# Kernel tuning notes

Hardware: AMD Instinct MI355X
Metric: run time of the kernel (lower is better)

## Reference

```python
import jax, jax.numpy as jnp
import numpy as np

DIM = 768
GP_NUM = 49


def setup_inputs() -> dict:
    key = jax.random.key(0)
    ks = jax.random.split(key, 7)
    b, n, d = 16, 1024, DIM
    s = d ** -0.5
    x = jax.random.normal(ks[0], (b, n, d), dtype=jnp.float32)
    W_qkv = jax.random.normal(ks[1], (d, 3 * d), dtype=jnp.float32) * s
    b_qkv = jnp.zeros((3 * d,), dtype=jnp.float32)
    W_proj = jax.random.normal(ks[2], (d, d), dtype=jnp.float32) * s
    b_proj = jnp.zeros((d,), dtype=jnp.float32)
    W_gp = jax.random.normal(ks[3], (d, GP_NUM), dtype=jnp.float32) * s
    alpha = jnp.zeros((1,), dtype=jnp.float32)
    return {"x": x, "W_qkv": W_qkv, "b_qkv": b_qkv, "W_proj": W_proj,
            "b_proj": b_proj, "W_gp": W_gp, "alpha": alpha}


def reference(x, W_qkv, b_qkv, W_proj, b_proj, W_gp, alpha):
    d = x.shape[-1]
    scale = d ** -0.5
    qkv = x @ W_qkv + b_qkv                      # (b, n, 3d)
    q, k, v = jnp.split(qkv, 3, axis=-1)
    scores = jnp.einsum('bnd,bmd->bnm', q, k) * scale
    attn = jax.nn.softmax(scores, axis=-1)       # (b, n, n)
    gw = jax.nn.softmax(q @ W_gp, axis=-1)       # (b, n, gp_num)
    group = jnp.einsum('bng,bmg->bnm', gw, gw)   # (b, n, n)
    a = jax.nn.sigmoid(alpha)                    # (1,)
    weights = attn * (a + (1.0 - a) * group)
    out = jnp.einsum('bnm,bmd->bnd', weights, v)
    return out @ W_proj + b_proj
```

## Files before the change

### kernel.cpp

```cpp
#include <hip/hip_runtime.h>
#include <stdint.h>

typedef __attribute__((ext_vector_type(8))) short short8;
typedef __attribute__((ext_vector_type(4))) short short4v;
typedef __attribute__((ext_vector_type(4))) float floatx4;
typedef _Float16 half2v __attribute__((ext_vector_type(2)));

__device__ __forceinline__ float b2f(unsigned short u) {
  union { unsigned int i; float f; } v; v.i = ((unsigned int)u) << 16; return v.f;
}
__device__ __forceinline__ unsigned short f2b(float f) {
  union { float f; unsigned int i; } v; v.f = f;
  unsigned int i = v.i;
  return (unsigned short)((i + 0x7FFFu + ((i >> 16) & 1u)) >> 16);
}
__device__ __forceinline__ short4v pack4(float a, float b, float c, float d) {
  short4v r;
  r[0] = (short)f2b(a); r[1] = (short)f2b(b); r[2] = (short)f2b(c); r[3] = (short)f2b(d);
  return r;
}

__device__ __forceinline__ void stage16(const unsigned short* g, unsigned short* lds_base) {
  __builtin_amdgcn_global_load_lds((__attribute__((address_space(1))) const unsigned int*)g,
                                   (__attribute__((address_space(3))) unsigned int*)lds_base,
                                   16, 0, 0);
}

template<int SYT, int SXT>
__global__ __launch_bounds__(256, 4) void gemm_bt(
    const unsigned short* __restrict__ A, const unsigned short* __restrict__ B,
    unsigned short* __restrict__ Cb, float* __restrict__ Cf,
    const float* __restrict__ rowdiv, const float* __restrict__ bias,
    int K, int lda, int ldb, int ldc,
    long long sA, long long sB, long long sC, long long sRD)
{
  const int tid  = threadIdx.x;
  const int lane = tid & 63;
  const int wave = tid >> 6;
  const int wr = wave >> 1, wc = wave & 1;
  int m0, n0;
  if constexpr (SYT > 0) {
    const int lin  = blockIdx.x;
    const int xcd  = lin & 7;
    const int rem  = lin >> 3;
    const int yloc = rem / SXT;
    const int x    = rem - yloc * SXT;
    m0 = (xcd * SYT + yloc) * 128;
    n0 = x * 128;
  } else {
    m0 = blockIdx.y * 128;
    n0 = blockIdx.x * 128;
  }
  const int bz = blockIdx.z;
  A += (long long)bz * sA;
  B += (long long)bz * sB;
  const float* rd = rowdiv ? rowdiv + (long long)bz * sRD : (const float*)0;

  __shared__ unsigned short As[128 * 32];
  __shared__ unsigned short Bs[128 * 32];

  floatx4 acc[4][4];
#pragma unroll
  for (int i = 0; i < 4; ++i)
#pragma unroll
    for (int j = 0; j < 4; ++j) acc[i][j] = floatx4{0.f, 0.f, 0.f, 0.f};

  const int t    = (lane & 7) ^ (lane >> 3);
  const int srow = 2 * (lane >> 3) + (t >> 2);
  const int scol = (t & 3) * 8;
  const unsigned short* ga0 = A + (long long)(m0 + wave * 32 + srow) * lda + scol;
  const unsigned short* ga1 = ga0 + 16LL * lda;
  const unsigned short* gb0 = B + (long long)(n0 + wave * 32 + srow) * ldb + scol;
  const unsigned short* gb1 = gb0 + 16LL * ldb;
  unsigned short* lA0 = As + wave * 1024;
  unsigned short* lA1 = lA0 + 512;
  unsigned short* lB0 = Bs + wave * 1024;
  unsigned short* lB1 = lB0 + 512;

  const int l15  = lane & 15;
  const int q    = lane >> 4;
  const int rofs = (l15 >> 1) * 64 + (((q + 4 * (l15 & 1)) ^ (l15 >> 1)) * 8);

  for (int kt = 0; kt < K; kt += 32) {
    __syncthreads();
    stage16(ga0 + kt, lA0);
    stage16(ga1 + kt, lA1);
    stage16(gb0 + kt, lB0);
    stage16(gb1 + kt, lB1);
    __syncthreads();
    short8 af[4], bfv[4];
#pragma unroll
    for (int i = 0; i < 4; ++i) af[i]  = *(const short8*)&As[(wr * 32 + i * 8) * 64 + rofs];
#pragma unroll
    for (int j = 0; j < 4; ++j) bfv[j] = *(const short8*)&Bs[(wc * 32 + j * 8) * 64 + rofs];
#pragma unroll
    for (int i = 0; i < 4; ++i)
#pragma unroll
      for (int j = 0; j < 4; ++j)
        acc[i][j] = __builtin_amdgcn_mfma_f32_16x16x32_bf16(bfv[j], af[i], acc[i][j], 0, 0, 0);
  }

#pragma unroll
  for (int i = 0; i < 4; ++i) {
    const int row = m0 + wr * 64 + i * 16 + l15;
    const float rcp = rd ? __builtin_amdgcn_rcpf(rd[row]) : 1.0f;
#pragma unroll
    for (int j = 0; j < 4; ++j) {
      const int colb = n0 + wc * 64 + j * 16 + q * 4;
      floatx4 v = acc[i][j];
      if (rd) { v[0] *= rcp; v[1] *= rcp; v[2] *= rcp; v[3] *= rcp; }
      if (bias) {
        const float4 bi = *(const float4*)&bias[colb];
        v[0] += bi.x; v[1] += bi.y; v[2] += bi.z; v[3] += bi.w;
      }
      if (Cb) *(short4v*)&Cb[(long long)bz * sC + (long long)row * ldc + colb] = pack4(v[0], v[1], v[2], v[3]);
      else    *(floatx4*)&Cf[(long long)bz * sC + (long long)row * ldc + colb] = v;
    }
  }
}

__global__ __launch_bounds__(256) void score_weights(
    const unsigned short* __restrict__ qkv, const unsigned short* __restrict__ gw,
    unsigned short* __restrict__ Wout, float* __restrict__ L,
    const float* __restrict__ alpha)
{
  const int tid  = threadIdx.x;
  const int lane = tid & 63;
  const int wave = tid >> 6;
  const int wr = wave >> 1, wc = wave & 1;
  const int n0 = blockIdx.x * 128;
  const int m0 = blockIdx.y * 128;
  const int b  = blockIdx.z;

  const int l15 = lane & 15;
  const int q   = lane >> 4;
  const int q8  = q * 8;

  const unsigned short* gq = gw + ((long long)(b * 1024 + m0 + wr * 64)) * 64;
  const unsigned short* gk = gw + ((long long)(b * 1024 + n0 + wc * 64)) * 64;
  floatx4 gacc[4][4];
#pragma unroll
  for (int i = 0; i < 4; ++i)
#pragma unroll
    for (int j = 0; j < 4; ++j) gacc[i][j] = floatx4{0.f, 0.f, 0.f, 0.f};
#pragma unroll
  for (int ks = 0; ks < 2; ++ks) {
    short8 af[4], bfv[4];
#pragma unroll
    for (int i = 0; i < 4; ++i) af[i]  = *(const short8*)&gq[(long long)(i * 16 + l15) * 64 + ks * 32 + q8];
#pragma unroll
    for (int j = 0; j < 4; ++j) bfv[j] = *(const short8*)&gk[(long long)(j * 16 + l15) * 64 + ks * 32 + q8];
#pragma unroll
    for (int i = 0; i < 4; ++i)
#pragma unroll
      for (int j = 0; j < 4; ++j)
        gacc[i][j] = __builtin_amdgcn_mfma_f32_16x16x32_bf16(bfv[j], af[i], gacc[i][j], 0, 0, 0);
  }
  const float aa    = 1.0f / (1.0f + __expf(-alpha[0]));
  const float onema = 1.0f - aa;
  half2v gfp[4][4][2];
#pragma unroll
  for (int i = 0; i < 4; ++i)
#pragma unroll
    for (int j = 0; j < 4; ++j) {
      gfp[i][j][0] = half2v{(_Float16)(aa + onema * gacc[i][j][0]),
                            (_Float16)(aa + onema * gacc[i][j][1])};
      gfp[i][j][1] = half2v{(_Float16)(aa + onema * gacc[i][j][2]),
                            (_Float16)(aa + onema * gacc[i][j][3])};
    }

  const unsigned short* Aq = qkv + ((long long)(b * 1024 + m0)) * 1536;
  const unsigned short* Bk = qkv + ((long long)(b * 1024 + n0)) * 1536 + 768;

  __shared__ unsigned short As[128 * 32];
  __shared__ unsigned short Bs[128 * 32];

  floatx4 sacc[4][4];
#pragma unroll
  for (int i = 0; i < 4; ++i)
#pragma unroll
    for (int j = 0; j < 4; ++j) sacc[i][j] = floatx4{0.f, 0.f, 0.f, 0.f};

  const int t    = (lane & 7) ^ (lane >> 3);
  const int srow = 2 * (lane >> 3) + (t >> 2);
  const int scol = (t & 3) * 8;
  const unsigned short* ga0 = Aq + (long long)(wave * 32 + srow) * 1536 + scol;
  const unsigned short* ga1 = ga0 + 16LL * 1536;
  const unsigned short* gb0 = Bk + (long long)(wave * 32 + srow) * 1536 + scol;
  const unsigned short* gb1 = gb0 + 16LL * 1536;
  unsigned short* lA0 = As + wave * 1024;
  unsigned short* lA1 = lA0 + 512;
  unsigned short* lB0 = Bs + wave * 1024;
  unsigned short* lB1 = lB0 + 512;

  const int rofs = (l15 >> 1) * 64 + (((q + 4 * (l15 & 1)) ^ (l15 >> 1)) * 8);

  for (int kt = 0; kt < 768; kt += 32) {
    __syncthreads();
    stage16(ga0 + kt, lA0);
    stage16(ga1 + kt, lA1);
    stage16(gb0 + kt, lB0);
    stage16(gb1 + kt, lB1);
    __syncthreads();
    short8 af[4], bfv[4];
#pragma unroll
    for (int i = 0; i < 4; ++i) af[i]  = *(const short8*)&As[(wr * 32 + i * 8) * 64 + rofs];
#pragma unroll
    for (int j = 0; j < 4; ++j) bfv[j] = *(const short8*)&Bs[(wc * 32 + j * 8) * 64 + rofs];
#pragma unroll
    for (int i = 0; i < 4; ++i)
#pragma unroll
      for (int j = 0; j < 4; ++j)
        sacc[i][j] = __builtin_amdgcn_mfma_f32_16x16x32_bf16(bfv[j], af[i], sacc[i][j], 0, 0, 0);
  }

  const float scale = 0.03608439182435161f;
  unsigned short* Wb = Wout + ((long long)b << 20);

#pragma unroll
  for (int i = 0; i < 4; ++i) {
    const int row = m0 + wr * 64 + i * 16 + l15;
    float ls = 0.0f;
#pragma unroll
    for (int j = 0; j < 4; ++j) {
      const int colb = n0 + wc * 64 + j * 16 + q * 4;
      float e0 = __expf(sacc[i][j][0] * scale);
      float e1 = __expf(sacc[i][j][1] * scale);
      float e2 = __expf(sacc[i][j][2] * scale);
      float e3 = __expf(sacc[i][j][3] * scale);
      ls += (e0 + e1) + (e2 + e3);
      *(short4v*)&Wb[(long long)row * 1024 + colb] =
        pack4(e0 * (float)gfp[i][j][0][0], e1 * (float)gfp[i][j][0][1],
              e2 * (float)gfp[i][j][1][0], e3 * (float)gfp[i][j][1][1]);
    }
    ls += __shfl_xor(ls, 16, 64);
    ls += __shfl_xor(ls, 32, 64);
    if (lane < 16) atomicAdd(&L[b * 1024 + row], ls);
  }
}

__global__ __launch_bounds__(256) void gw_mfma(
    const unsigned short* __restrict__ qkv, const unsigned short* __restrict__ Wgp64,
    unsigned short* __restrict__ gw)
{
  const int lane = threadIdx.x & 63;
  const int wave = threadIdx.x >> 6;
  const int l15  = lane & 15;
  const int q    = lane >> 4;
  const int q8   = q * 8;
  const long long row0 = (long long)blockIdx.x * 64 + wave * 16;
  const unsigned short* A = qkv + row0 * 1536;

  floatx4 acc[4];
#pragma unroll
  for (int j = 0; j < 4; ++j) acc[j] = floatx4{0.f, 0.f, 0.f, 0.f};

  for (int kt = 0; kt < 768; kt += 32) {
    short8 af = *(const short8*)&A[(long long)l15 * 1536 + kt + q8];
    short8 bf[4];
#pragma unroll
    for (int j = 0; j < 4; ++j)
      bf[j] = *(const short8*)&Wgp64[(j * 16 + l15) * 768 + kt + q8];
#pragma unroll
    for (int j = 0; j < 4; ++j)
      acc[j] = __builtin_amdgcn_mfma_f32_16x16x32_bf16(bf[j], af, acc[j], 0, 0, 0);
  }

  float mx = -1e30f;
#pragma unroll
  for (int j = 0; j < 4; ++j)
#pragma unroll
    for (int e = 0; e < 4; ++e) {
      const int col = j * 16 + q * 4 + e;
      if (col < 49) mx = fmaxf(mx, acc[j][e]);
    }
  mx = fmaxf(mx, __shfl_xor(mx, 16, 64));
  mx = fmaxf(mx, __shfl_xor(mx, 32, 64));

  float ev[4][4];
  float s = 0.0f;
#pragma unroll
  for (int j = 0; j < 4; ++j)
#pragma unroll
    for (int e = 0; e < 4; ++e) {
      const int col = j * 16 + q * 4 + e;
      const float x = (col < 49) ? __expf(acc[j][e] - mx) : 0.0f;
      ev[j][e] = x;
      s += x;
    }
  s += __shfl_xor(s, 16, 64);
  s += __shfl_xor(s, 32, 64);
  const float inv = 1.0f / s;

  unsigned short* out = gw + (row0 + l15) * 64;
#pragma unroll
  for (int j = 0; j < 4; ++j)
    *(short4v*)&out[j * 16 + q * 4] =
      pack4(ev[j][0] * inv, ev[j][1] * inv, ev[j][2] * inv, ev[j][3] * inv);
}

__global__ __launch_bounds__(256) void small_gemm_nt(
    const unsigned short* __restrict__ A, const unsigned short* __restrict__ B,
    unsigned short* __restrict__ C)
{
  const int lane = threadIdx.x & 63;
  const int wave = threadIdx.x >> 6;
  const int l15  = lane & 15;
  const int q    = lane >> 4;
  const int q8   = q * 8;
  const int rows0 = (blockIdx.y * 4 + wave) * 16;
  const int cols0 = blockIdx.x * 64;

  floatx4 acc[4];
#pragma unroll
  for (int j = 0; j < 4; ++j) acc[j] = floatx4{0.f, 0.f, 0.f, 0.f};

  for (int kt = 0; kt < 768; kt += 32) {
    short8 af = *(const short8*)&A[(rows0 + l15) * 768 + kt + q8];
    short8 bf[4];
#pragma unroll
    for (int j = 0; j < 4; ++j)
      bf[j] = *(const short8*)&B[(cols0 + j * 16 + l15) * 768 + kt + q8];
#pragma unroll
    for (int j = 0; j < 4; ++j)
      acc[j] = __builtin_amdgcn_mfma_f32_16x16x32_bf16(bf[j], af, acc[j], 0, 0, 0);
  }

  unsigned short* out = C + (rows0 + l15) * 768 + cols0;
#pragma unroll
  for (int j = 0; j < 4; ++j)
    *(short4v*)&out[j * 16 + q * 4] = pack4(acc[j][0], acc[j][1], acc[j][2], acc[j][3]);
}

__global__ void convert_f2b(const float* __restrict__ in, unsigned short* __restrict__ out, long long n)
{
  long long i = ((long long)blockIdx.x * 256 + threadIdx.x) * 4;
  if (i + 3 >= n) {
    for (long long k = i; k < n; ++k) out[k] = f2b(in[k]);
    return;
  }
  float4 v = *(const float4*)(in + i);
  out[i + 0] = f2b(v.x);
  out[i + 1] = f2b(v.y);
  out[i + 2] = f2b(v.z);
  out[i + 3] = f2b(v.w);
}

__global__ void transpose_f2b(const float* __restrict__ in, unsigned short* __restrict__ out,
                              int R, int C, int ldin, int ldout)
{
  __shared__ unsigned short t[32][33];
  const int c0 = blockIdx.x * 32, r0 = blockIdx.y * 32;
  for (int i = threadIdx.y; i < 32; i += 8) {
    const int r = r0 + i, c = c0 + threadIdx.x;
    if (r < R && c < C) t[i][threadIdx.x] = f2b(in[(long long)r * ldin + c]);
  }
  __syncthreads();
  for (int i = threadIdx.y; i < 32; i += 8) {
    const int r = c0 + i, c = r0 + threadIdx.x;
    if (r < C && c < R) out[(long long)r * ldout + c] = t[threadIdx.x][i];
  }
}

__global__ void slice_f2b(const float* __restrict__ in, unsigned short* __restrict__ out)
{
  const long long idx = (long long)blockIdx.x * 256 + threadIdx.x;
  const int r = (int)(idx / 768), c = (int)(idx - (long long)r * 768);
  out[idx] = f2b(in[(long long)r * 2304 + 1536 + c]);
}

__global__ __launch_bounds__(256) void bias2_kernel(
    const unsigned short* __restrict__ WprojT, const float* __restrict__ b_qkv,
    const float* __restrict__ b_proj, float* __restrict__ bias2)
{
  const int lane = threadIdx.x & 63;
  const int wave = threadIdx.x >> 6;
  const int j = blockIdx.x * 4 + wave;
  float s = 0.0f;
#pragma unroll
  for (int tt = 0; tt < 12; ++tt) {
    const int d = tt * 64 + lane;
    s += b2f(WprojT[j * 768 + d]) * b_qkv[1536 + d];
  }
#pragma unroll
  for (int m = 1; m < 64; m <<= 1) s += __shfl_xor(s, m, 64);
  if (lane == 0) bias2[j] = b_proj[j] + s;
}

extern "C" void kernel_launch(void* const* d_in, const int* in_sizes, int n_in,
                              void* d_out, int out_size, void* d_ws, size_t ws_size,
                              hipStream_t stream)
{
  const float* x      = (const float*)d_in[0];
  const float* W_qkv  = (const float*)d_in[1];
  const float* b_qkv  = (const float*)d_in[2];
  const float* W_proj = (const float*)d_in[3];
  const float* b_proj = (const float*)d_in[4];
  const float* W_gp   = (const float*)d_in[5];
  const float* alpha  = (const float*)d_in[6];

  char* p = (char*)d_ws;
  auto alloc = [&](size_t bytes) { char* r = p; p += (bytes + 255) & ~255ULL; return r; };
  unsigned short* qk     = (unsigned short*)alloc(16384ULL * 1536 * 2);
  unsigned short* xb     = (unsigned short*)alloc(16384ULL * 768 * 2);
  unsigned short* WqkvT  = (unsigned short*)alloc(1536ULL * 768 * 2);
  unsigned short* WprojT = (unsigned short*)alloc(768ULL * 768 * 2);
  unsigned short* WvB    = (unsigned short*)alloc(768ULL * 768 * 2);
  unsigned short* Wcomb  = (unsigned short*)alloc(768ULL * 768 * 2);
  unsigned short* Wgp64  = (unsigned short*)alloc(64ULL * 768 * 2);
  unsigned short* gwbuf  = (unsigned short*)alloc(16384ULL * 64 * 2);
  float*          Lbuf   = (float*)alloc(16384ULL * 4);
  float*          bias2  = (float*)alloc(768ULL * 4);
  unsigned short* wmat   = (unsigned short*)alloc(16ULL * 1024 * 1024 * 2);
  unsigned short* vpT    = (unsigned short*)alloc(16ULL * 768 * 1024 * 2);

  const dim3 blk256(256);
  const dim3 tb(32, 8);

  convert_f2b<<<dim3(12288), blk256, 0, stream>>>(x, xb, 16384LL * 768);
  transpose_f2b<<<dim3(48, 24), tb, 0, stream>>>(W_qkv, WqkvT, 768, 1536, 2304, 768);
  transpose_f2b<<<dim3(24, 24), tb, 0, stream>>>(W_proj, WprojT, 768, 768, 768, 768);
  hipMemsetAsync(Wgp64, 0, 64ULL * 768 * 2, stream);
  transpose_f2b<<<dim3(2, 24), tb, 0, stream>>>(W_gp, Wgp64, 768, 49, 49, 768);
  slice_f2b<<<dim3(2304), blk256, 0, stream>>>(W_qkv, WvB);

  small_gemm_nt<<<dim3(12, 12), blk256, 0, stream>>>(WprojT, WvB, Wcomb);
  bias2_kernel<<<dim3(192), blk256, 0, stream>>>(WprojT, b_qkv, b_proj, bias2);

  gemm_bt<16, 12><<<dim3(1536, 1, 1), blk256, 0, stream>>>(xb, WqkvT, qk, (float*)0,
                                                           (const float*)0, b_qkv,
                                                           768, 768, 768, 1536, 0, 0, 0, 0);

  gw_mfma<<<dim3(256), blk256, 0, stream>>>(qk, Wgp64, gwbuf);

  hipMemsetAsync(Lbuf, 0, 16384 * 4, stream);

  score_weights<<<dim3(8, 8, 16), blk256, 0, stream>>>(qk, gwbuf, wmat, Lbuf, alpha);

  gemm_bt<0, 0><<<dim3(8, 6, 16), blk256, 0, stream>>>(Wcomb, xb, vpT, (float*)0,
                                                       (const float*)0, (const float*)0,
                                                       768, 768, 768, 1024,
                                                       0, 1024LL * 768, 768LL * 1024, 0);

  gemm_bt<0, 0><<<dim3(6, 8, 16), blk256, 0, stream>>>(wmat, vpT, (unsigned short*)0, (float*)d_out,
                                                       Lbuf, bias2,
                                                       1024, 1024, 1024, 768,
                                                       1024LL * 1024, 768LL * 1024, 1024LL * 768, 1024);
}
```

Measured before the change: 366.8 us.

## Split QKV GEMM between 128-tile kernel and new 256x256-tile 512-thread kernel

Adds a 256x256-tile GEMM kernel with 512 threads, a 4-stage global_load_lds pipeline and XCD-aware block mapping. The QKV projection is split in half: the first 8192 rows still use the existing 128-tile kernel, and the second half uses the new large-tile kernel. Larger tiles raise data reuse per LDS load, but they also mean fewer blocks (192) and higher register and LDS pressure, and the two halves run one after the other on the stream.

```diff
diff --git a/kernel.cpp b/kernel.cpp
--- a/kernel.cpp
+++ b/kernel.cpp
@@ -119,6 +119,125 @@
   }
 }
 
+template<int SYT, int SXT>
+__global__ __launch_bounds__(512, 1) void gemm256d(
+    const unsigned short* __restrict__ A, const unsigned short* __restrict__ B,
+    unsigned short* __restrict__ Cb, float* __restrict__ Cf,
+    const float* __restrict__ rowdiv, const float* __restrict__ bias,
+    int K, int lda, int ldb, int ldc,
+    long long sA, long long sB, long long sC, long long sRD)
+{
+  const int tid  = threadIdx.x;
+  const int lane = tid & 63;
+  const int wave = tid >> 6;
+  const int wr = wave >> 2;
+  const int wc = wave & 3;
+  int m0, n0;
+  if constexpr (SYT > 0) {
+    const int lin  = blockIdx.x;
+    const int xcd  = lin & 7;
+    const int rem  = lin >> 3;
+    const int yloc = rem / SXT;
+    const int x    = rem - yloc * SXT;
+    m0 = (xcd * SYT + yloc) * 256;
+    n0 = x * 256;
+  } else {
+    m0 = blockIdx.y * 256;
+    n0 = blockIdx.x * 256;
+  }
+  const int bz = blockIdx.z;
+  A += (long long)bz * sA;
+  B += (long long)bz * sB;
+  const float* rd = rowdiv ? rowdiv + (long long)bz * sRD : (const float*)0;
+
+  __shared__ __align__(16) unsigned short lds[4 * 16384];
+
+  floatx4 acc[8][4];
+#pragma unroll
+  for (int i = 0; i < 8; ++i)
+#pragma unroll
+    for (int j = 0; j < 4; ++j) acc[i][j] = floatx4{0.f, 0.f, 0.f, 0.f};
+
+  const int t    = (lane & 7) ^ (lane >> 3);
+  const int srow = 2 * (lane >> 3) + (t >> 2);
+  const int scol = (t & 3) * 8;
+  const unsigned short* ga0 = A + (long long)(m0 + wave * 32 + srow) * lda + scol;
+  const unsigned short* ga1 = ga0 + 16LL * lda;
+  const unsigned short* gb0 = B + (long long)(n0 + wave * 32 + srow) * ldb + scol;
+  const unsigned short* gb1 = gb0 + 16LL * ldb;
+
+  const int l15  = lane & 15;
+  const int q    = lane >> 4;
+  const int rofs = (l15 >> 1) * 64 + (((q + 4 * (l15 & 1)) ^ (l15 >> 1)) * 8);
+
+  short8 af8[8], bfv[4];
+
+  auto STAGE = [&](int kt, int buf) {
+    unsigned short* dA = lds + buf * 16384 + wave * 1024;
+    unsigned short* dB = dA + 8192;
+    stage16(ga0 + kt, dA);
+    stage16(ga1 + kt, dA + 512);
+    stage16(gb0 + kt, dB);
+    stage16(gb1 + kt, dB + 512);
+  };
+  auto READ_ALL = [&](int buf) {
+    const unsigned short* Ab = lds + buf * 16384;
+    const unsigned short* Bb = Ab + 8192;
+#pragma unroll
+    for (int j = 0; j < 4; ++j)
+      bfv[j] = *(const short8*)&Bb[(wc * 32 + j * 8) * 64 + rofs];
+#pragma unroll
+    for (int i = 0; i < 8; ++i)
+      af8[i] = *(const short8*)&Ab[(wr * 64 + i * 8) * 64 + rofs];
+  };
+  auto MFMA32 = [&]() {
+#pragma unroll
+    for (int i = 0; i < 8; ++i)
+#pragma unroll
+      for (int j = 0; j < 4; ++j)
+        acc[i][j] = __builtin_amdgcn_mfma_f32_16x16x32_bf16(bfv[j], af8[i], acc[i][j], 0, 0, 0);
+  };
+
+  const int nt = K >> 5;
+
+  STAGE(0, 0);
+  STAGE(32, 1);
+  STAGE(64, 2);
+  asm volatile("s_waitcnt vmcnt(8)" ::: "memory");
+  __builtin_amdgcn_s_barrier();
+
+  for (int tt = 0; tt < nt; ++tt) {
+    const int buf = tt & 3;
+    if (tt + 3 < nt) STAGE((tt + 3) << 5, (tt + 3) & 3);
+    READ_ALL(buf);
+    __builtin_amdgcn_s_setprio(1);
+    MFMA32();
+    __builtin_amdgcn_s_setprio(0);
+    if (tt < nt - 3)       { asm volatile("s_waitcnt vmcnt(8)" ::: "memory"); }
+    else if (tt == nt - 3) { asm volatile("s_waitcnt vmcnt(4)" ::: "memory"); }
+    else if (tt == nt - 2) { asm volatile("s_waitcnt vmcnt(0)" ::: "memory"); }
+    if (tt + 1 < nt) __builtin_amdgcn_s_barrier();
+  }
+
+#pragma unroll
+  for (int i = 0; i < 8; ++i) {
+    const int row = m0 + wr * 128 + i * 16 + l15;
+    const float rcp = rd ? __builtin_amdgcn_rcpf(rd[row]) : 1.0f;
+#pragma unroll
+    for (int j = 0; j < 4; ++j) {
+      const int colb = n0 + wc * 64 + j * 16 + q * 4;
+      floatx4 v = acc[i][j];
+      if (rd) { v[0] *= rcp; v[1] *= rcp; v[2] *= rcp; v[3] *= rcp; }
+      if (bias) {
+        const float4 bi = *(const float4*)&bias[colb];
+        v[0] += bi.x; v[1] += bi.y; v[2] += bi.z; v[3] += bi.w;
+      }
+      if (Cb) *(short4v*)&Cb[(long long)bz * sC + (long long)row * ldc + colb] = pack4(v[0], v[1], v[2], v[3]);
+      else    *(floatx4*)&Cf[(long long)bz * sC + (long long)row * ldc + colb] = v;
+    }
+  }
+}
+
 __global__ __launch_bounds__(256) void score_weights(
     const unsigned short* __restrict__ qkv, const unsigned short* __restrict__ gw,
     unsigned short* __restrict__ Wout, float* __restrict__ L,
@@ -415,6 +534,7 @@
   unsigned short* vpT    = (unsigned short*)alloc(16ULL * 768 * 1024 * 2);
 
   const dim3 blk256(256);
+  const dim3 blk512(512);
   const dim3 tb(32, 8);
 
   convert_f2b<<<dim3(12288), blk256, 0, stream>>>(x, xb, 16384LL * 768);
@@ -427,9 +547,13 @@
   small_gemm_nt<<<dim3(12, 12), blk256, 0, stream>>>(WprojT, WvB, Wcomb);
   bias2_kernel<<<dim3(192), blk256, 0, stream>>>(WprojT, b_qkv, b_proj, bias2);
 
-  gemm_bt<16, 12><<<dim3(1536, 1, 1), blk256, 0, stream>>>(xb, WqkvT, qk, (float*)0,
-                                                           (const float*)0, b_qkv,
-                                                           768, 768, 768, 1536, 0, 0, 0, 0);
+  gemm_bt<8, 12><<<dim3(768, 1, 1), blk256, 0, stream>>>(xb, WqkvT, qk, (float*)0,
+                                                         (const float*)0, b_qkv,
+                                                         768, 768, 768, 1536, 0, 0, 0, 0);
+  gemm256d<4, 6><<<dim3(192, 1, 1), blk512, 0, stream>>>(xb + 8192LL * 768, WqkvT,
+                                                         qk + 8192LL * 1536, (float*)0,
+                                                         (const float*)0, b_qkv,
+                                                         768, 768, 768, 1536, 0, 0, 0, 0);
 
   gw_mfma<<<dim3(256), blk256, 0, stream>>>(qk, Wgp64, gwbuf);
 
```

Result: no change. 373.4 us (+1.8%).
